# Kernel optimization log

Hardware: AMD Instinct MI355X
Metric: run time of the kernel (lower is better)

The kernel has to match this reference:

```python
import jax, jax.numpy as jnp
import numpy as np

T = 128        # number of timesteps (init arg T)
LEN_M = 32     # causal window length (init arg len_M)
N = 8192       # nodes
F = 64         # features per node


def setup_inputs() -> dict:
    key = jax.random.key(0)
    k1, k2, k3 = jax.random.split(key, 3)
    X = jax.random.normal(k1, (T, N, F), dtype=jnp.float32)
    # M_pad[r] holds the length-(r+1) parameter M[str(r+1)] in its first r+1 slots
    # (padding is masked out before softmax, so its values are irrelevant).
    M_pad = jax.random.normal(k2, (LEN_M, LEN_M), dtype=jnp.float32)
    # M_big[j] corresponds to parameter key str(LEN_M+1+j); keys LEN_M+1..T-1 are
    # used by rows LEN_M+1..T-1 (row LEN_M reuses M[str(LEN_M)] = M_pad[-1], per the source).
    M_big = jax.random.normal(k3, (T - LEN_M - 1, LEN_M), dtype=jnp.float32)
    return {"X": X, "M_pad": M_pad, "M_big": M_big}


def _band_weights(M_pad, M_big):
    """Build the [T, T] causal banded mixing matrix with per-row softmax weights."""
    cols = jnp.arange(LEN_M)
    # rows 0..LEN_M-1: softmax over the growing prefix window of length row+1
    prefix_mask = cols[None, :] <= jnp.arange(LEN_M)[:, None]            # [LEN_M, LEN_M]
    w_small = jax.nn.softmax(jnp.where(prefix_mask, M_pad, -jnp.inf), axis=1)
    # rows LEN_M..T-1 use key str(row): row==LEN_M reuses M_pad[-1], rest use M_big
    logits_big = jnp.concatenate([M_pad[LEN_M - 1:LEN_M], M_big], axis=0)  # [T-LEN_M, LEN_M]
    w_big = jax.nn.softmax(logits_big, axis=1)
    W = jnp.zeros((T, T), dtype=M_pad.dtype)
    W = W.at[:LEN_M, :LEN_M].set(w_small)  # w_small is zero outside the prefix window
    rows = jnp.arange(LEN_M, T)
    cidx = (rows - LEN_M + 1)[:, None] + cols[None, :]  # sliding window cols per row
    W = W.at[rows[:, None], cidx].set(w_big)
    return W


def reference(X, M_pad, M_big):
    W = _band_weights(M_pad, M_big)          # [T, T] banded
    data = X.reshape(T, -1)                  # [T, N*F]
    out = W @ data                           # causal windowed weighted sum, all rows at once
    return out.reshape(X.shape)
```

## Files before the change

### kernel.cpp

```cpp
#include <hip/hip_runtime.h>
#include <math.h>

#define T_    128
#define LENM  32
#define NCOL  (8192 * 64)

typedef float f2_t __attribute__((ext_vector_type(2)));

__global__ void build_w_kernel(const float* __restrict__ M_pad,
                               const float* __restrict__ M_big,
                               float* __restrict__ Wc) {
    int t = threadIdx.x;
    if (t >= T_) return;
    const float* src;
    int len, joff;
    if (t < LENM)       { src = M_pad + t * LENM;              len = t + 1; joff = LENM - 1 - t; }
    else if (t == LENM) { src = M_pad + (LENM - 1) * LENM;     len = LENM;  joff = 0; }
    else                { src = M_big + (t - LENM - 1) * LENM; len = LENM;  joff = 0; }

    float m = -3.4e38f;
    for (int j = 0; j < len; ++j) m = fmaxf(m, src[j]);
    float e[LENM];
    float s = 0.f;
    for (int j = 0; j < len; ++j) { e[j] = expf(src[j] - m); s += e[j]; }
    float inv = 1.f / s;
    for (int j = 0; j < LENM; ++j) Wc[t * LENM + j] = 0.f;
    for (int j = 0; j < len; ++j)  Wc[t * LENM + joff + j] = e[j] * inv;
}

typedef float f4_t __attribute__((ext_vector_type(4)));

template<int R>
__device__ __forceinline__ void step(const f2_t* __restrict__ xp,
                                     f2_t* __restrict__ op,
                                     const f4_t* w4,
                                     f2_t (&A)[LENM], f2_t (&B)[LENM]) {
    constexpr int K     = R / LENM;
    constexpr int i_    = R % LENM;
    constexpr int jmin_ = (R < LENM) ? (LENM - 1 - i_) : 0;
    f2_t (&CUR)[LENM] = (K & 1) ? B : A;
    f2_t (&PRV)[LENM] = (K & 1) ? A : B;
    const size_t rs = NCOL / 2;

    if constexpr (R + 8 < T_) {
        f2_t ld = xp[(size_t)(R + 8) * rs];
        if constexpr (i_ < LENM - 8) CUR[i_ + 8] = ld;
        else                         PRV[i_ - (LENM - 8)] = ld;
    }

    f2_t acc; acc.x = 0.f; acc.y = 0.f;
#pragma unroll
    for (int q = 0; q < 8; ++q) {
        if (q * 4 + 3 >= jmin_) {
            f4_t w = w4[R * 8 + q];
#pragma unroll
            for (int m = 0; m < 4; ++m) {
                const int j = q * 4 + m;
                if (j >= jmin_) {
                    f2_t xv = (j < LENM - 1 - i_) ? PRV[i_ + 1 + j]
                                                  : CUR[i_ + j - (LENM - 1)];
                    float wm = (m == 0) ? w.x : (m == 1) ? w.y
                             : (m == 2) ? w.z : w.w;
                    acc.x = fmaf(wm, xv.x, acc.x);
                    acc.y = fmaf(wm, xv.y, acc.y);
                }
            }
        }
    }
    __builtin_nontemporal_store(acc, &op[(size_t)R * rs]);
}

template<int R>
__device__ __forceinline__ void run_steps(const f2_t* __restrict__ xp,
                                          f2_t* __restrict__ op,
                                          const f4_t* w4,
                                          f2_t (&A)[LENM], f2_t (&B)[LENM]) {
    if constexpr (R < T_) {
        step<R>(xp, op, w4, A, B);
        run_steps<R + 1>(xp, op, w4, A, B);
    }
}

__global__ __launch_bounds__(256, 4) void band_mix_kernel(
    const float* __restrict__ X,
    const float* __restrict__ Wc,
    float* __restrict__ out) {
    __shared__ f4_t w4[T_ * LENM / 4];
    for (int i = threadIdx.x; i < T_ * LENM / 4; i += 256)
        w4[i] = reinterpret_cast<const f4_t*>(Wc)[i];
    __syncthreads();

    const int c = (blockIdx.x * 256 + threadIdx.x) * 2;
    const f2_t* xp = reinterpret_cast<const f2_t*>(X + c);
    f2_t* op = reinterpret_cast<f2_t*>(out + c);
    const size_t rs = NCOL / 2;

    f2_t A[LENM], B[LENM];
#pragma unroll
    for (int i = 0; i < 8; ++i) A[i] = xp[(size_t)i * rs];

    run_steps<0>(xp, op, w4, A, B);
}

extern "C" void kernel_launch(void* const* d_in, const int* in_sizes, int n_in,
                              void* d_out, int out_size, void* d_ws, size_t ws_size,
                              hipStream_t stream) {
    const float* X     = (const float*)d_in[0];
    const float* M_pad = (const float*)d_in[1];
    const float* M_big = (const float*)d_in[2];
    float* out = (float*)d_out;
    float* Wc  = (float*)d_ws;

    build_w_kernel<<<1, 128, 0, stream>>>(M_pad, M_big, Wc);
    band_mix_kernel<<<NCOL / 2 / 256, 256, 0, stream>>>(X, Wc, out);
}
```

Before: 101.3 us.

## Split time axis into chunks with halo reload to increase block parallelism

Each block now processes one of four 32-row time chunks for its column group instead of all 128 rows, with a 40-slot circular register window. Chunks after the first reload a 31-row halo of preceding inputs. This raises grid size and shortens per-thread serial work, and the smaller register window may improve occupancy, at the cost of extra global reads for the halo rows.

```diff
diff --git a/kernel.cpp b/kernel.cpp
--- a/kernel.cpp
+++ b/kernel.cpp
@@ -1,11 +1,16 @@
 #include <hip/hip_runtime.h>
 #include <math.h>
 
-#define T_    128
-#define LENM  32
-#define NCOL  (8192 * 64)
+#define T_     128
+#define LENM   32
+#define NCOL   (8192 * 64)
+#define WSLOTS 40
+#define LA     8
+#define CHROWS 32
+#define NCHUNK (T_ / CHROWS)
 
 typedef float f2_t __attribute__((ext_vector_type(2)));
+typedef float f4_t __attribute__((ext_vector_type(4)));
 
 __global__ void build_w_kernel(const float* __restrict__ M_pad,
                                const float* __restrict__ M_big,
@@ -28,26 +33,28 @@
     for (int j = 0; j < len; ++j)  Wc[t * LENM + joff + j] = e[j] * inv;
 }
 
-typedef float f4_t __attribute__((ext_vector_type(4)));
 
-template<int R>
-__device__ __forceinline__ void step(const f2_t* __restrict__ xp,
-                                     f2_t* __restrict__ op,
-                                     const f4_t* w4,
-                                     f2_t (&A)[LENM], f2_t (&B)[LENM]) {
-    constexpr int K     = R / LENM;
-    constexpr int i_    = R % LENM;
-    constexpr int jmin_ = (R < LENM) ? (LENM - 1 - i_) : 0;
-    f2_t (&CUR)[LENM] = (K & 1) ? B : A;
-    f2_t (&PRV)[LENM] = (K & 1) ? A : B;
-    const size_t rs = NCOL / 2;
+template<int C, int ROW>
+__device__ __forceinline__ void load_in(const f2_t* __restrict__ xp,
+                                        f2_t (&WIN)[WSLOTS]) {
+    WIN[(ROW - C * CHROWS + (LENM - 1)) % WSLOTS] = xp[(size_t)ROW * (NCOL / 2)];
+}
 
-    if constexpr (R + 8 < T_) {
-        f2_t ld = xp[(size_t)(R + 8) * rs];
-        if constexpr (i_ < LENM - 8) CUR[i_ + 8] = ld;
-        else                         PRV[i_ - (LENM - 8)] = ld;
+template<int C, int R0, int CNT>
+__device__ __forceinline__ void load_seq(const f2_t* __restrict__ xp,
+                                         f2_t (&WIN)[WSLOTS]) {
+    if constexpr (CNT > 0) {
+        load_in<C, R0>(xp, WIN);
+        load_seq<C, R0 + 1, CNT - 1>(xp, WIN);
     }
+}
 
+template<int C, int I>
+__device__ __forceinline__ void comp_row(f2_t* __restrict__ op,
+                                         const f4_t* w4,
+                                         const f2_t (&WIN)[WSLOTS]) {
+    constexpr int R     = C * CHROWS + I;
+    constexpr int jmin_ = (R < LENM) ? (LENM - 1 - R) : 0;
     f2_t acc; acc.x = 0.f; acc.y = 0.f;
 #pragma unroll
     for (int q = 0; q < 8; ++q) {
@@ -57,8 +64,7 @@
             for (int m = 0; m < 4; ++m) {
                 const int j = q * 4 + m;
                 if (j >= jmin_) {
-                    f2_t xv = (j < LENM - 1 - i_) ? PRV[i_ + 1 + j]
-                                                  : CUR[i_ + j - (LENM - 1)];
+                    f2_t xv = WIN[(I + j) % WSLOTS];
                     float wm = (m == 0) ? w.x : (m == 1) ? w.y
                              : (m == 2) ? w.z : w.w;
                     acc.x = fmaf(wm, xv.x, acc.x);
@@ -67,18 +73,30 @@
             }
         }
     }
-    __builtin_nontemporal_store(acc, &op[(size_t)R * rs]);
+    __builtin_nontemporal_store(acc, &op[(size_t)R * (NCOL / 2)]);
 }
 
-template<int R>
+template<int C, int I>
 __device__ __forceinline__ void run_steps(const f2_t* __restrict__ xp,
                                           f2_t* __restrict__ op,
                                           const f4_t* w4,
-                                          f2_t (&A)[LENM], f2_t (&B)[LENM]) {
-    if constexpr (R < T_) {
-        step<R>(xp, op, w4, A, B);
-        run_steps<R + 1>(xp, op, w4, A, B);
+                                          f2_t (&WIN)[WSLOTS]) {
+    if constexpr (I < CHROWS) {
+        if constexpr (I + LA < CHROWS)
+            load_in<C, C * CHROWS + I + LA>(xp, WIN);
+        comp_row<C, I>(op, w4, WIN);
+        run_steps<C, I + 1>(xp, op, w4, WIN);
     }
+}
+
+template<int C>
+__device__ __forceinline__ void run_chunk(const f2_t* __restrict__ xp,
+                                          f2_t* __restrict__ op,
+                                          const f4_t* w4,
+                                          f2_t (&WIN)[WSLOTS]) {
+    if constexpr (C == 0) load_seq<0, 0, LA>(xp, WIN);
+    else                  load_seq<C, C * CHROWS - (LENM - 1), (LENM - 1) + LA>(xp, WIN);
+    run_steps<C, 0>(xp, op, w4, WIN);
 }
 
 __global__ __launch_bounds__(256, 4) void band_mix_kernel(
@@ -90,16 +108,19 @@
         w4[i] = reinterpret_cast<const f4_t*>(Wc)[i];
     __syncthreads();
 
-    const int c = (blockIdx.x * 256 + threadIdx.x) * 2;
+    const int ch     = blockIdx.x & (NCHUNK - 1);
+    const int colgrp = blockIdx.x >> 2;
+    const int c = (colgrp * 256 + threadIdx.x) * 2;
     const f2_t* xp = reinterpret_cast<const f2_t*>(X + c);
     f2_t* op = reinterpret_cast<f2_t*>(out + c);
-    const size_t rs = NCOL / 2;
 
-    f2_t A[LENM], B[LENM];
-#pragma unroll
-    for (int i = 0; i < 8; ++i) A[i] = xp[(size_t)i * rs];
-
-    run_steps<0>(xp, op, w4, A, B);
+    f2_t WIN[WSLOTS];
+    switch (ch) {
+        case 0: run_chunk<0>(xp, op, w4, WIN); break;
+        case 1: run_chunk<1>(xp, op, w4, WIN); break;
+        case 2: run_chunk<2>(xp, op, w4, WIN); break;
+        case 3: run_chunk<3>(xp, op, w4, WIN); break;
+    }
 }
 
 extern "C" void kernel_launch(void* const* d_in, const int* in_sizes, int n_in,
@@ -112,5 +133,5 @@
     float* Wc  = (float*)d_ws;
 
     build_w_kernel<<<1, 128, 0, stream>>>(M_pad, M_big, Wc);
-    band_mix_kernel<<<NCOL / 2 / 256, 256, 0, stream>>>(X, Wc, out);
+    band_mix_kernel<<<(NCOL / 2 / 256) * NCHUNK, 256, 0, stream>>>(X, Wc, out);
 }
```

Result: slower. 142.1 us (+40.3%).
